# Kernel optimization log

Measured on AMD Instinct MI355X. Metric: run time of the kernel, lower is better.

## Reference

```python
import jax, jax.numpy as jnp
import numpy as np
import math

T, B, E, H, NEXP = 512, 8, 1024, 32, 256
DH = E // H
S = T + NEXP
SCALING = (DH / 1) ** 0.5 / DH  # = 1/sqrt(head_dim) for d_tilde=1
LN_EPS = 1e-5


def _xavier(key, shape, gain):
    fan_in, fan_out = shape[1], shape[0]
    a = gain * math.sqrt(6.0 / (fan_in + fan_out))
    return jax.random.uniform(key, shape, jnp.float32, -a, a)


def setup_inputs() -> dict:
    key = jax.random.key(0)
    ks = jax.random.split(key, 12)
    g = 1.0 / math.sqrt(2.0)  # xavier gain 1/sqrt(2*d_tilde)
    return {
        "query": jax.random.normal(ks[0], (T, B, E), jnp.float32),
        "attn_bias": jax.random.normal(ks[1], (B * H, T, S), jnp.float32) * 0.1,
        "outcell_index": jax.random.randint(ks[2], (B, NEXP), 0, T - 1),
        "expand_mask": jax.random.randint(ks[3], (B, NEXP), 0, 2).astype(bool),
        "key_padding_mask": jnp.zeros((B, T), bool),
        "Wq": _xavier(ks[4], (E, E), g),
        "bq": jnp.zeros((E,), jnp.float32),
        "Wk": _xavier(ks[5], (E, E), g),  # k_proj has no bias (k_bias=False)
        "Wv": _xavier(ks[6], (E, E), g),
        "bv": jnp.zeros((E,), jnp.float32),
        "Wo": _xavier(ks[7], (E, E), 1.0),
        "bo": jnp.zeros((E,), jnp.float32),
        "ln_g": jnp.ones((E,), jnp.float32),
        "ln_b": jnp.zeros((E,), jnp.float32),
    }


def reference(query, attn_bias, outcell_index, expand_mask, key_padding_mask,
              Wq, bq, Wk, Wv, bv, Wo, bo, ln_g, ln_b):
    # projections (Time x Batch x Channel)
    q = (query @ Wq.T + bq) * SCALING          # [T,B,E]
    k = query @ Wk.T                            # [T,B,E] (no bias)
    v = query @ Wv.T + bv                       # [T,B,E]

    # PBC gather-expansion of K/V along time dim (note +1 offset as in source)
    idx = outcell_index.T + 1                   # [NEXP,B]
    idx3 = jnp.broadcast_to(idx[:, :, None], (NEXP, B, E))
    expand_k = jnp.take_along_axis(k, idx3, axis=0)
    expand_v = jnp.take_along_axis(v, idx3, axis=0)
    k = jnp.concatenate([k, expand_k], axis=0)  # [S,B,E]
    v = jnp.concatenate([v, expand_v], axis=0)  # [S,B,E]

    # split heads
    qh = q.reshape(T, B, H, DH)
    kh = k.reshape(S, B, H, DH)
    vh = v.reshape(S, B, H, DH)

    scores = jnp.einsum("tbhd,sbhd->bhts", qh, kh)  # [B,H,T,S]
    scores = scores + attn_bias.reshape(B, H, T, S)

    mask = jnp.concatenate([key_padding_mask, expand_mask], axis=1)  # [B,S]
    scores = jnp.where(mask[:, None, None, :], -jnp.inf, scores)

    probs = jax.nn.softmax(scores, axis=-1)      # [B,H,T,S]

    attn = jnp.einsum("bhts,sbhd->tbhd", probs, vh).reshape(T, B, E)

    # layer norm then output projection
    mu = attn.mean(-1, keepdims=True)
    var = ((attn - mu) ** 2).mean(-1, keepdims=True)
    attn = (attn - mu) * jax.lax.rsqrt(var + LN_EPS) * ln_g + ln_b
    out = attn @ Wo.T + bo                       # [T,B,E]

    attn_weights_mean = probs.mean(axis=1)       # [B,T,S] (mean over heads)
    return out, attn_weights_mean
```

## Files before the change

### kernel.cpp

```cpp
#include <hip/hip_runtime.h>

#define DEV __device__ __forceinline__

typedef short bh8 __attribute__((ext_vector_type(8)));
typedef short bh4 __attribute__((ext_vector_type(4)));
typedef float fx4 __attribute__((ext_vector_type(4)));

#define T_ 512
#define B_ 8
#define E_ 1024
#define H_ 32
#define DH_ 32
#define S_ 768
#define NEXP_ 256
#define SCALING_ 0.17677669529663687f
#define OFF_QB    ((size_t)0)
#define OFF_WB    ((size_t)8388608)
#define OFF_QRM   ((size_t)16777216)
#define OFF_KRM   ((size_t)25165824)
#define OFF_VRM   ((size_t)33554432)
#define OFF_KBF   ((size_t)41943040)
#define OFF_VT    ((size_t)54525952)
#define OFF_ATTN  ((size_t)67108864)
#define OFF_XHAT  ((size_t)75497472)
#define OFF_MASK  ((size_t)83886080)
#define OFF_FLAG  ((size_t)83910656)
#define OFF_MEANP ((size_t)100663296)
#define SLAB_ ((size_t)B_ * T_ * S_)

#define BARRIER_LGKM() do { \
  asm volatile("s_waitcnt lgkmcnt(0)" ::: "memory"); \
  __builtin_amdgcn_s_barrier(); \
} while (0)

#define WAIT_VM0_BARRIER() do { \
  asm volatile("s_waitcnt vmcnt(0) lgkmcnt(0)" ::: "memory"); \
  __builtin_amdgcn_s_barrier(); \
} while (0)

DEV float bf2f(short u) {
  union { unsigned int i; float f; } x;
  x.i = ((unsigned int)(unsigned short)u) << 16;
  return x.f;
}
DEV short f2bf(float f) {
  union { float f; unsigned int u; } x; x.f = f;
  unsigned int r = x.u + 0x7fffu + ((x.u >> 16) & 1u);
  return (short)(r >> 16);
}
DEV void gl_lds16(const void* g, void* l) {
  __builtin_amdgcn_global_load_lds(
      (const __attribute__((address_space(1))) unsigned int*)g,
      (__attribute__((address_space(3))) unsigned int*)l, 16, 0, 0);
}

__global__ __launch_bounds__(256) void conv_all(
    const float* __restrict__ q, const float* __restrict__ wq,
    const float* __restrict__ wk, const float* __restrict__ wv,
    const float* __restrict__ wo, short* __restrict__ QB, short* __restrict__ WB,
    const unsigned char* __restrict__ em, int* __restrict__ flag) {
  if (blockIdx.x == 0) {
    __shared__ int f;
    if (threadIdx.x == 0) f = 0;
    __syncthreads();
    for (int i = threadIdx.x; i < 2048; i += 256)
      if ((i & 3) && em[i]) atomicOr(&f, 1);
    __syncthreads();
    if (threadIdx.x == 0) *flag = f;
  }
  size_t i4 = ((size_t)blockIdx.x * 256 + threadIdx.x) * 4;
  const float* s; short* d;
  if (i4 < (size_t)4194304) { s = q + i4; d = QB + i4; }
  else {
    size_t r = i4 - 4194304; int m = (int)(r >> 20); size_t o = r & 1048575;
    const float* ws4[4] = {wq, wk, wv, wo};
    s = ws4[m] + o; d = WB + ((size_t)m << 20) + o;
  }
  fx4 v = *(const fx4*)s;
  bh4 p = { f2bf(v[0]), f2bf(v[1]), f2bf(v[2]), f2bf(v[3]) };
  *(bh4*)d = p;
}

__global__ __launch_bounds__(256) void qkv_gemm(
    const short* __restrict__ QB, const short* __restrict__ WB,
    const float* __restrict__ bq, const float* __restrict__ bv,
    short* __restrict__ q_rm, short* __restrict__ k_rm, short* __restrict__ v_rm) {
  __shared__ __align__(16) short As[128 * 32];
  __shared__ __align__(16) short Ws[128 * 32];
  const int tid = threadIdx.x;
  const int mt = blockIdx.x, nt = blockIdx.y;
  const int mat = nt >> 3;
  const size_t m0 = (size_t)mt * 128;
  const int n0 = (nt & 7) << 7;
  const short* W = WB + (size_t)mat * (1024 * 1024);
  const int l = tid & 63, wv_ = tid >> 6;
  const int lt = l & 15, g = l >> 4;
  const int wm = wv_ >> 1, wn = wv_ & 1;
  fx4 acc[4][4];
#pragma unroll
  for (int i = 0; i < 4; ++i)
#pragma unroll
    for (int j = 0; j < 4; ++j) acc[i][j] = fx4{0.f, 0.f, 0.f, 0.f};

  const int r0 = tid >> 2, c0 = tid & 3;
  for (int kt = 0; kt < 32; ++kt) {
    const int k0 = kt * 32;
    __syncthreads();
    gl_lds16(QB + (m0 + r0) * 1024 + k0 + c0 * 8,        As + r0 * 32 + c0 * 8);
    gl_lds16(QB + (m0 + 64 + r0) * 1024 + k0 + c0 * 8,   As + (64 + r0) * 32 + c0 * 8);
    gl_lds16(W + (size_t)(n0 + r0) * 1024 + k0 + c0 * 8,      Ws + r0 * 32 + c0 * 8);
    gl_lds16(W + (size_t)(n0 + 64 + r0) * 1024 + k0 + c0 * 8, Ws + (64 + r0) * 32 + c0 * 8);
    __syncthreads();
    bh8 af[4], wf[4];
#pragma unroll
    for (int i = 0; i < 4; ++i) af[i] = *(const bh8*)(As + (wm * 64 + i * 16 + lt) * 32 + g * 8);
#pragma unroll
    for (int j = 0; j < 4; ++j) wf[j] = *(const bh8*)(Ws + (wn * 64 + j * 16 + lt) * 32 + g * 8);
#pragma unroll
    for (int i = 0; i < 4; ++i)
#pragma unroll
      for (int j = 0; j < 4; ++j)
        acc[i][j] = __builtin_amdgcn_mfma_f32_16x16x32_bf16(af[i], wf[j], acc[i][j], 0, 0, 0);
  }
  short* outp = (mat == 0) ? q_rm : (mat == 1) ? k_rm : v_rm;
#pragma unroll
  for (int i = 0; i < 4; ++i) {
    const size_t rowb = m0 + wm * 64 + i * 16 + g * 4;
#pragma unroll
    for (int j = 0; j < 4; ++j) {
      const int col = n0 + wn * 64 + j * 16 + lt;
      const float bias = (mat == 0) ? bq[col] : (mat == 2) ? bv[col] : 0.0f;
#pragma unroll
      for (int jj = 0; jj < 4; ++jj) {
        float v = acc[i][j][jj] + bias;
        if (mat == 0) v *= SCALING_;
        outp[(rowb + jj) * 1024 + col] = f2bf(v);
      }
    }
  }
}

__global__ __launch_bounds__(256) void repack(
    const short* __restrict__ k_rm, const short* __restrict__ v_rm,
    const int* __restrict__ oc, const unsigned char* __restrict__ em,
    const unsigned char* __restrict__ kp, const int* __restrict__ flag,
    short* __restrict__ kbf, short* __restrict__ vT, float* __restrict__ maskval) {
  __shared__ __align__(16) short lv[2][64 * 40];
  const int bid = blockIdx.x, tid = threadIdx.x;
  if (bid < 768) {
#pragma unroll
    for (int k = 0; k < 4; ++k) {
      int u = bid * 1024 + k * 256 + tid;
      int d8 = u & 3;
      int s = (u >> 2) % 768;
      int hb = (u >> 2) / 768;
      int b = hb >> 5, h = hb & 31;
      int srct = (s < 512) ? s : (oc[b * 256 + (s - 512)] + 1);
      bh8 val = *(const bh8*)(k_rm + ((size_t)srct * 8 + b) * 1024 + h * 32 + d8 * 8);
      *(bh8*)(kbf + ((size_t)hb * 768 + s) * 32 + d8 * 8) = val;
    }
  } else if (bid < 2304) {
    int idx2 = bid - 768;
    int s_loc = tid >> 2, d8 = tid & 3;
#pragma unroll
    for (int k = 0; k < 2; ++k) {
      int chunk = idx2 * 2 + k;
      int c = chunk % 12, hb = chunk / 12;
      int b = hb >> 5, h = hb & 31;
      int s = c * 64 + s_loc;
      int srct = (s < 512) ? s : (oc[b * 256 + (s - 512)] + 1);
      bh8 val = *(const bh8*)(v_rm + ((size_t)srct * 8 + b) * 1024 + h * 32 + d8 * 8);
      *(bh8*)(lv[k] + s_loc * 40 + d8 * 8) = val;
    }
    __syncthreads();
    int d = tid >> 3, sj = tid & 7;
#pragma unroll
    for (int k = 0; k < 2; ++k) {
      int chunk = idx2 * 2 + k;
      int c = chunk % 12, hb = chunk / 12;
      bh8 o;
#pragma unroll
      for (int e = 0; e < 8; ++e) o[e] = lv[k][(sj * 8 + e) * 40 + d];
      *(bh8*)(vT + ((size_t)hb * 32 + d) * 768 + c * 64 + sj * 8) = o;
    }
  } else {
    int u = (bid - 2304) * 256 + tid;
    if (u < 6144) {
      int s = u % 768, b = u / 768;
      int m;
      if (*flag) {
        m = (s < 512) ? (int)kp[b * 512 + s] : (int)em[b * 256 + (s - 512)];
      } else {
        const int* kpi = (const int*)kp; const int* emi = (const int*)em;
        m = (s < 512) ? kpi[b * 512 + s] : emi[b * 256 + (s - 512)];
      }
      maskval[u] = m ? -3.0e38f : 0.0f;
    }
  }
}

__global__ __launch_bounds__(256) void attn_kernel(
    const short* __restrict__ q_rm, const short* __restrict__ kbf,
    const short* __restrict__ vT, const float* __restrict__ bias,
    const float* __restrict__ maskval, short* __restrict__ attn_bf,
    float* __restrict__ mean_part) {
  __shared__ __align__(16) float bias_lds[16 * 768];
  __shared__ __align__(16) short p_st[4 * 16 * 40];
  __shared__ float lpart[4][16];
  __shared__ __align__(16) float attred[4 * 64 * 8];
  __shared__ __align__(16) float maskv[768];

  const int tid = threadIdx.x, blk = blockIdx.x;
  const int group = blk & 15, tt = blk >> 4;
  const int hg = group & 1, b = group >> 1;
  const int t0 = tt * 16;
  const int w = tid >> 6, l = tid & 63, lt = l & 15, g = l >> 4;
  const int sbase = w * 192;

  for (int u = tid; u < 768; u += 256) maskv[u] = maskval[b * 768 + u];

  const float* bias_base = bias + ((size_t)(b * 32) * 512 + t0) * 768;
  {
    const float* hb_ = bias_base + (size_t)(hg * 16) * 512 * 768;
#pragma unroll
    for (int r = 0; r < 12; ++r)
      gl_lds16(hb_ + (size_t)(r * 256 + tid) * 4,
               (char*)bias_lds + (size_t)(r * 256 + tid) * 16);
  }
  WAIT_VM0_BARRIER();

  const fx4 zf = {0.f, 0.f, 0.f, 0.f};
  float msum[48];
#pragma unroll
  for (int i = 0; i < 48; ++i) msum[i] = 0.f;

  for (int i = 0; i < 16; ++i) {
    const int hh = hg * 16 + i;
    const int bh = b * 32 + hh;

    const bh8 qf = *(const bh8*)(q_rm + ((size_t)(t0 + lt) * 8 + b) * 1024 + hh * 32 + g * 8);
    const short* kp_ = kbf + (size_t)bh * 768 * 32;

    unsigned exu[24];
    float ls0 = 0.f, ls1 = 0.f, ls2 = 0.f, ls3 = 0.f;
#pragma unroll
    for (int c = 0; c < 12; ++c) {
      const int s0 = sbase + c * 16;
      bh8 kf = *(const bh8*)(kp_ + (s0 + lt) * 32 + g * 8);
      fx4 sc = __builtin_amdgcn_mfma_f32_16x16x32_bf16(qf, kf, zf, 0, 0, 0);
      const float mv = maskv[s0 + lt];
      const float* bl = bias_lds + (g * 4) * 768 + s0 + lt;
      float e0 = __expf(sc[0] + bl[0]       + mv);
      float e1 = __expf(sc[1] + bl[768]     + mv);
      float e2 = __expf(sc[2] + bl[2 * 768] + mv);
      float e3 = __expf(sc[3] + bl[3 * 768] + mv);
      ls0 += e0; ls1 += e1; ls2 += e2; ls3 += e3;
      exu[c * 2]     = (unsigned)(unsigned short)f2bf(e0) | ((unsigned)(unsigned short)f2bf(e1) << 16);
      exu[c * 2 + 1] = (unsigned)(unsigned short)f2bf(e2) | ((unsigned)(unsigned short)f2bf(e3) << 16);
    }
#pragma unroll
    for (int m = 1; m < 16; m <<= 1) {
      ls0 += __shfl_xor(ls0, m); ls1 += __shfl_xor(ls1, m);
      ls2 += __shfl_xor(ls2, m); ls3 += __shfl_xor(ls3, m);
    }
    if (lt == 0) {
      lpart[w][g * 4 + 0] = ls0; lpart[w][g * 4 + 1] = ls1;
      lpart[w][g * 4 + 2] = ls2; lpart[w][g * 4 + 3] = ls3;
    }
    BARRIER_LGKM();

    if (i < 15) {
      const float* hb_ = bias_base + (size_t)(hh + 1) * 512 * 768;
#pragma unroll
      for (int r = 0; r < 12; ++r)
        gl_lds16(hb_ + (size_t)(r * 256 + tid) * 4,
                 (char*)bias_lds + (size_t)(r * 256 + tid) * 16);
    }

    float linv[4];
#pragma unroll
    for (int jj = 0; jj < 4; ++jj)
      linv[jj] = 1.0f / (lpart[0][g * 4 + jj] + lpart[1][g * 4 + jj] +
                         lpart[2][g * 4 + jj] + lpart[3][g * 4 + jj]);
    const float linv_acc = 1.0f / (lpart[0][lt] + lpart[1][lt] + lpart[2][lt] + lpart[3][lt]);

    fx4 acc0 = zf, acc1 = zf;
    const short* vp0 = vT + ((size_t)bh * 32 + lt) * 768;
    const short* vp1 = vp0 + 16 * 768;
    short* pw_base = p_st + w * 640;
#pragma unroll
    for (int c2 = 0; c2 < 6; ++c2) {
      const int s0 = sbase + c2 * 32;
#pragma unroll
      for (int cc = 0; cc < 2; ++cc) {
        const int c = c2 * 2 + cc;
        unsigned u01 = exu[c * 2], u23 = exu[c * 2 + 1];
        short* pcol = pw_base + cc * 16 + lt;
        pcol[(g * 4 + 0) * 40] = (short)(u01 & 0xffffu);
        pcol[(g * 4 + 1) * 40] = (short)(u01 >> 16);
        pcol[(g * 4 + 2) * 40] = (short)(u23 & 0xffffu);
        pcol[(g * 4 + 3) * 40] = (short)(u23 >> 16);
        msum[c * 4 + 0] += bf2f((short)(u01 & 0xffffu)) * linv[0];
        msum[c * 4 + 1] += bf2f((short)(u01 >> 16)) * linv[1];
        msum[c * 4 + 2] += bf2f((short)(u23 & 0xffffu)) * linv[2];
        msum[c * 4 + 3] += bf2f((short)(u23 >> 16)) * linv[3];
      }
      bh8 pf = *(const bh8*)(pw_base + lt * 40 + g * 8);
      bh8 vf0 = *(const bh8*)(vp0 + s0 + g * 8);
      bh8 vf1 = *(const bh8*)(vp1 + s0 + g * 8);
      acc0 = __builtin_amdgcn_mfma_f32_16x16x32_bf16(vf0, pf, acc0, 0, 0, 0);
      acc1 = __builtin_amdgcn_mfma_f32_16x16x32_bf16(vf1, pf, acc1, 0, 0, 0);
    }
#pragma unroll
    for (int jj = 0; jj < 4; ++jj) { acc0[jj] *= linv_acc; acc1[jj] *= linv_acc; }

    float* ar = attred + (w * 64 + l) * 8;
    *(fx4*)(ar) = acc0;
    *(fx4*)(ar + 4) = acc1;
    BARRIER_LGKM();
    if (w < 2) {
      float s0v = 0.f, s1v = 0.f, s2v = 0.f, s3v = 0.f;
#pragma unroll
      for (int w2 = 0; w2 < 4; ++w2) {
        const float* a2 = attred + (w2 * 64 + l) * 8 + w * 4;
        s0v += a2[0]; s1v += a2[1]; s2v += a2[2]; s3v += a2[3];
      }
      bh4 o = { f2bf(s0v), f2bf(s1v), f2bf(s2v), f2bf(s3v) };
      *(bh4*)(attn_bf + ((size_t)(t0 + lt) * 8 + b) * 1024 + hh * 32 + w * 16 + g * 4) = o;
    }
    WAIT_VM0_BARRIER();
  }

  float* mob = mean_part + (size_t)hg * SLAB_ + ((size_t)b * 512 + t0) * 768;
#pragma unroll
  for (int c = 0; c < 12; ++c) {
    const int s = sbase + c * 16 + lt;
#pragma unroll
    for (int jj = 0; jj < 4; ++jj) {
      mob[(size_t)(g * 4 + jj) * 768 + s] = msum[c * 4 + jj] * 0.03125f;
    }
  }
}

__global__ __launch_bounds__(256) void mean_ln(
    const float* __restrict__ mean_part, float* __restrict__ mean_out,
    const short* __restrict__ attn_bf, const float* __restrict__ lg,
    const float* __restrict__ lb, short* __restrict__ xhat) {
  if (blockIdx.x < 3072) {
    size_t i = ((size_t)blockIdx.x * 256 + threadIdx.x) * 4;
    fx4 a = *(const fx4*)(mean_part + i);
    fx4 b = *(const fx4*)(mean_part + SLAB_ + i);
#pragma unroll
    for (int k = 0; k < 4; ++k) a[k] = a[k] + b[k];
    *(fx4*)(mean_out + i) = a;
    return;
  }
  const int w = threadIdx.x >> 6, l = threadIdx.x & 63;
  const size_t row = (size_t)(blockIdx.x - 3072) * 4 + w;
  const short* x = attn_bf + row * 1024 + l * 16;
  bh8 a0 = *(const bh8*)x, a1 = *(const bh8*)(x + 8);
  float xs[16];
#pragma unroll
  for (int i = 0; i < 8; ++i) { xs[i] = bf2f(a0[i]); xs[8 + i] = bf2f(a1[i]); }
  float s1 = 0.f, s2 = 0.f;
#pragma unroll
  for (int i = 0; i < 16; ++i) { s1 += xs[i]; s2 += xs[i] * xs[i]; }
  for (int m = 1; m < 64; m <<= 1) { s1 += __shfl_xor(s1, m); s2 += __shfl_xor(s2, m); }
  const float mu = s1 * (1.0f / 1024.0f);
  float var = s2 * (1.0f / 1024.0f) - mu * mu;
  var = fmaxf(var, 0.f);
  const float rs = rsqrtf(var + 1e-5f);
  const float* lgp = lg + l * 16;
  const float* lbp = lb + l * 16;
  bh8 o0, o1;
#pragma unroll
  for (int i = 0; i < 8; ++i) {
    o0[i] = f2bf((xs[i] - mu) * rs * lgp[i] + lbp[i]);
    o1[i] = f2bf((xs[8 + i] - mu) * rs * lgp[8 + i] + lbp[8 + i]);
  }
  short* y = xhat + row * 1024 + l * 16;
  *(bh8*)y = o0;
  *(bh8*)(y + 8) = o1;
}

__global__ __launch_bounds__(256) void out_gemm(
    const short* __restrict__ XH, const short* __restrict__ WoB,
    const float* __restrict__ bo, float* __restrict__ out) {
  __shared__ __align__(16) short As[128 * 32];
  __shared__ __align__(16) short Ws[128 * 32];
  const int tid = threadIdx.x;
  const int mt = blockIdx.x, nt = blockIdx.y;
  const size_t m0 = (size_t)mt * 128;
  const int n0 = nt << 7;
  const int l = tid & 63, wv_ = tid >> 6;
  const int lt = l & 15, g = l >> 4;
  const int wm = wv_ >> 1, wn = wv_ & 1;
  fx4 acc[4][4];
#pragma unroll
  for (int i = 0; i < 4; ++i)
#pragma unroll
    for (int j = 0; j < 4; ++j) acc[i][j] = fx4{0.f, 0.f, 0.f, 0.f};
  const int r0 = tid >> 2, c0 = tid & 3;
  for (int kt = 0; kt < 32; ++kt) {
    const int k0 = kt * 32;
    __syncthreads();
    gl_lds16(XH + (m0 + r0) * 1024 + k0 + c0 * 8,        As + r0 * 32 + c0 * 8);
    gl_lds16(XH + (m0 + 64 + r0) * 1024 + k0 + c0 * 8,   As + (64 + r0) * 32 + c0 * 8);
    gl_lds16(WoB + (size_t)(n0 + r0) * 1024 + k0 + c0 * 8,      Ws + r0 * 32 + c0 * 8);
    gl_lds16(WoB + (size_t)(n0 + 64 + r0) * 1024 + k0 + c0 * 8, Ws + (64 + r0) * 32 + c0 * 8);
    __syncthreads();
    bh8 af[4], wf[4];
#pragma unroll
    for (int i = 0; i < 4; ++i) af[i] = *(const bh8*)(As + (wm * 64 + i * 16 + lt) * 32 + g * 8);
#pragma unroll
    for (int j = 0; j < 4; ++j) wf[j] = *(const bh8*)(Ws + (wn * 64 + j * 16 + lt) * 32 + g * 8);
#pragma unroll
    for (int i = 0; i < 4; ++i)
#pragma unroll
      for (int j = 0; j < 4; ++j)
        acc[i][j] = __builtin_amdgcn_mfma_f32_16x16x32_bf16(af[i], wf[j], acc[i][j], 0, 0, 0);
  }
#pragma unroll
  for (int i = 0; i < 4; ++i) {
    const size_t rowb = m0 + wm * 64 + i * 16 + g * 4;
#pragma unroll
    for (int j = 0; j < 4; ++j) {
      const int col = n0 + wn * 64 + j * 16 + lt;
      const float bb = bo[col];
#pragma unroll
      for (int jj = 0; jj < 4; ++jj)
        out[(rowb + jj) * 1024 + col] = acc[i][j][jj] + bb;
    }
  }
}

extern "C" void kernel_launch(void* const* d_in, const int* in_sizes, int n_in,
                              void* d_out, int out_size, void* d_ws, size_t ws_size,
                              hipStream_t stream) {
  const float* query = (const float*)d_in[0];
  const float* attn_bias = (const float*)d_in[1];
  const int* oc = (const int*)d_in[2];
  const unsigned char* em = (const unsigned char*)d_in[3];
  const unsigned char* kp = (const unsigned char*)d_in[4];
  const float* Wq = (const float*)d_in[5];
  const float* bq = (const float*)d_in[6];
  const float* Wk = (const float*)d_in[7];
  const float* Wv = (const float*)d_in[8];
  const float* bv = (const float*)d_in[9];
  const float* Wo = (const float*)d_in[10];
  const float* bo = (const float*)d_in[11];
  const float* lg = (const float*)d_in[12];
  const float* lb = (const float*)d_in[13];

  char* w = (char*)d_ws;
  short* QB    = (short*)(w + OFF_QB);
  short* WB    = (short*)(w + OFF_WB);
  short* QRM   = (short*)(w + OFF_QRM);
  short* KRM   = (short*)(w + OFF_KRM);
  short* VRM   = (short*)(w + OFF_VRM);
  short* KBF   = (short*)(w + OFF_KBF);
  short* VT    = (short*)(w + OFF_VT);
  short* ATTN  = (short*)(w + OFF_ATTN);
  short* XHAT  = (short*)(w + OFF_XHAT);
  float* MASK  = (float*)(w + OFF_MASK);
  int*   FLAG  = (int*)(w + OFF_FLAG);
  float* MEANP = (float*)(w + OFF_MEANP);

  float* out0 = (float*)d_out;
  float* mean_out = out0 + (size_t)T_ * B_ * E_;

  conv_all<<<8192, 256, 0, stream>>>(query, Wq, Wk, Wv, Wo, QB, WB, em, FLAG);
  qkv_gemm<<<dim3(32, 24), 256, 0, stream>>>(QB, WB, bq, bv, QRM, KRM, VRM);
  repack<<<2328, 256, 0, stream>>>(KRM, VRM, oc, em, kp, FLAG, KBF, VT, MASK);
  attn_kernel<<<512, 256, 0, stream>>>(QRM, KBF, VT, attn_bias, MASK, ATTN, MEANP);
  mean_ln<<<4096, 256, 0, stream>>>(MEANP, mean_out, ATTN, lg, lb, XHAT);
  out_gemm<<<dim3(32, 8), 256, 0, stream>>>(XHAT, WB + (size_t)3 * 1024 * 1024, bo, out0);
}
```

Before: 242.8 us.

## Give each wave its own bias slice to drop per-head vmcnt barrier waits

The attention kernel now stages per-wave private bias slices (each wave loads only the 192 columns it consumes) instead of a block-shared 16x768 tile. Because each wave owns its data, the end-of-head barrier no longer waits on vmcnt, and a per-wave vmcnt wait at the top of the next head is enough. The next head's bias prefetch is issued earlier, right after the exp phase, and the first half of the V fragments are hoisted before the reduction barrier to overlap their latency. This trades some extra VGPRs for holding the prefetched V fragments, and it depends on the per-wave waitcnt discipline being correct.

```diff
diff --git a/kernel.cpp b/kernel.cpp
--- a/kernel.cpp
+++ b/kernel.cpp
@@ -33,11 +33,6 @@
   __builtin_amdgcn_s_barrier(); \
 } while (0)
 
-#define WAIT_VM0_BARRIER() do { \
-  asm volatile("s_waitcnt vmcnt(0) lgkmcnt(0)" ::: "memory"); \
-  __builtin_amdgcn_s_barrier(); \
-} while (0)
-
 DEV float bf2f(short u) {
   union { unsigned int i; float f; } x;
   x.i = ((unsigned int)(unsigned short)u) << 16;
@@ -204,7 +199,7 @@
     const short* __restrict__ vT, const float* __restrict__ bias,
     const float* __restrict__ maskval, short* __restrict__ attn_bf,
     float* __restrict__ mean_part) {
-  __shared__ __align__(16) float bias_lds[16 * 768];
+  __shared__ __align__(16) float bias_lds[4][16][192];
   __shared__ __align__(16) short p_st[4 * 16 * 40];
   __shared__ float lpart[4][16];
   __shared__ __align__(16) float attred[4 * 64 * 8];
@@ -220,23 +215,33 @@
   for (int u = tid; u < 768; u += 256) maskv[u] = maskval[b * 768 + u];
 
   const float* bias_base = bias + ((size_t)(b * 32) * 512 + t0) * 768;
-  {
-    const float* hb_ = bias_base + (size_t)(hg * 16) * 512 * 768;
-#pragma unroll
-    for (int r = 0; r < 12; ++r)
-      gl_lds16(hb_ + (size_t)(r * 256 + tid) * 4,
-               (char*)bias_lds + (size_t)(r * 256 + tid) * 16);
-  }
-  WAIT_VM0_BARRIER();
+#define STAGE_OWN(hh_) do { \
+    const float* hb_ = bias_base + (size_t)(hh_) * 512 * 768; \
+    _Pragma("unroll") \
+    for (int rr = 0; rr < 12; ++rr) { \
+      int gidx = rr * 64 + l; \
+      int row_ = gidx / 48, grp_ = gidx - row_ * 48; \
+      gl_lds16(hb_ + (size_t)row_ * 768 + sbase + grp_ * 4, \
+               (char*)bias_lds + (size_t)w * 12288 + (size_t)gidx * 16); \
+    } \
+  } while (0)
+
+  STAGE_OWN(hg * 16);
+  asm volatile("s_waitcnt vmcnt(0) lgkmcnt(0)" ::: "memory");
+  __builtin_amdgcn_s_barrier();
 
   const fx4 zf = {0.f, 0.f, 0.f, 0.f};
   float msum[48];
 #pragma unroll
   for (int i = 0; i < 48; ++i) msum[i] = 0.f;
+
+  const float* blkb = &bias_lds[w][0][0];
 
   for (int i = 0; i < 16; ++i) {
     const int hh = hg * 16 + i;
     const int bh = b * 32 + hh;
+
+    asm volatile("s_waitcnt vmcnt(0)" ::: "memory");
 
     const bh8 qf = *(const bh8*)(q_rm + ((size_t)(t0 + lt) * 8 + b) * 1024 + hh * 32 + g * 8);
     const short* kp_ = kbf + (size_t)bh * 768 * 32;
@@ -249,15 +254,27 @@
       bh8 kf = *(const bh8*)(kp_ + (s0 + lt) * 32 + g * 8);
       fx4 sc = __builtin_amdgcn_mfma_f32_16x16x32_bf16(qf, kf, zf, 0, 0, 0);
       const float mv = maskv[s0 + lt];
-      const float* bl = bias_lds + (g * 4) * 768 + s0 + lt;
+      const float* bl = blkb + (g * 4) * 192 + c * 16 + lt;
       float e0 = __expf(sc[0] + bl[0]       + mv);
-      float e1 = __expf(sc[1] + bl[768]     + mv);
-      float e2 = __expf(sc[2] + bl[2 * 768] + mv);
-      float e3 = __expf(sc[3] + bl[3 * 768] + mv);
+      float e1 = __expf(sc[1] + bl[192]     + mv);
+      float e2 = __expf(sc[2] + bl[2 * 192] + mv);
+      float e3 = __expf(sc[3] + bl[3 * 192] + mv);
       ls0 += e0; ls1 += e1; ls2 += e2; ls3 += e3;
       exu[c * 2]     = (unsigned)(unsigned short)f2bf(e0) | ((unsigned)(unsigned short)f2bf(e1) << 16);
       exu[c * 2 + 1] = (unsigned)(unsigned short)f2bf(e2) | ((unsigned)(unsigned short)f2bf(e3) << 16);
     }
+    asm volatile("s_waitcnt lgkmcnt(0)" ::: "memory");
+
+    const short* vp0 = vT + ((size_t)bh * 32 + lt) * 768;
+    const short* vp1 = vp0 + 16 * 768;
+    bh8 vf[6];
+#pragma unroll
+    for (int c2 = 0; c2 < 3; ++c2) {
+      vf[c2 * 2]     = *(const bh8*)(vp0 + sbase + c2 * 32 + g * 8);
+      vf[c2 * 2 + 1] = *(const bh8*)(vp1 + sbase + c2 * 32 + g * 8);
+    }
+    if (i < 15) STAGE_OWN(hh + 1);
+
 #pragma unroll
     for (int m = 1; m < 16; m <<= 1) {
       ls0 += __shfl_xor(ls0, m); ls1 += __shfl_xor(ls1, m);
@@ -268,15 +285,6 @@
       lpart[w][g * 4 + 2] = ls2; lpart[w][g * 4 + 3] = ls3;
     }
     BARRIER_LGKM();
-
-    if (i < 15) {
-      const float* hb_ = bias_base + (size_t)(hh + 1) * 512 * 768;
-#pragma unroll
-      for (int r = 0; r < 12; ++r)
-        gl_lds16(hb_ + (size_t)(r * 256 + tid) * 4,
-                 (char*)bias_lds + (size_t)(r * 256 + tid) * 16);
-    }
-
     float linv[4];
 #pragma unroll
     for (int jj = 0; jj < 4; ++jj)
@@ -285,8 +293,6 @@
     const float linv_acc = 1.0f / (lpart[0][lt] + lpart[1][lt] + lpart[2][lt] + lpart[3][lt]);
 
     fx4 acc0 = zf, acc1 = zf;
-    const short* vp0 = vT + ((size_t)bh * 32 + lt) * 768;
-    const short* vp1 = vp0 + 16 * 768;
     short* pw_base = p_st + w * 640;
 #pragma unroll
     for (int c2 = 0; c2 < 6; ++c2) {
@@ -306,8 +312,8 @@
         msum[c * 4 + 3] += bf2f((short)(u23 >> 16)) * linv[3];
       }
       bh8 pf = *(const bh8*)(pw_base + lt * 40 + g * 8);
-      bh8 vf0 = *(const bh8*)(vp0 + s0 + g * 8);
-      bh8 vf1 = *(const bh8*)(vp1 + s0 + g * 8);
+      bh8 vf0 = (c2 < 3) ? vf[c2 * 2]     : *(const bh8*)(vp0 + s0 + g * 8);
+      bh8 vf1 = (c2 < 3) ? vf[c2 * 2 + 1] : *(const bh8*)(vp1 + s0 + g * 8);
       acc0 = __builtin_amdgcn_mfma_f32_16x16x32_bf16(vf0, pf, acc0, 0, 0, 0);
       acc1 = __builtin_amdgcn_mfma_f32_16x16x32_bf16(vf1, pf, acc1, 0, 0, 0);
     }
@@ -328,7 +334,7 @@
       bh4 o = { f2bf(s0v), f2bf(s1v), f2bf(s2v), f2bf(s3v) };
       *(bh4*)(attn_bf + ((size_t)(t0 + lt) * 8 + b) * 1024 + hh * 32 + w * 16 + g * 4) = o;
     }
-    WAIT_VM0_BARRIER();
+    BARRIER_LGKM();
   }
 
   float* mob = mean_part + (size_t)hg * SLAB_ + ((size_t)b * 512 + t0) * 768;
@@ -340,6 +346,7 @@
       mob[(size_t)(g * 4 + jj) * 768 + s] = msum[c * 4 + jj] * 0.03125f;
     }
   }
+#undef STAGE_OWN
 }
 
 __global__ __launch_bounds__(256) void mean_ln(
```

Measured after the change: 263.2 us. +8.4%, slower.
